# Kernel optimization log

Measured on AMD Instinct MI355X. Metric: run time of the kernel, lower is better.

## Reference

```python
import jax, jax.numpy as jnp
import numpy as np

N_NODES = 20000
N_EDGES = 160000
D = 1000          # out_channels of GatedGraphConv / Linear in-dim
NUM_LAYERS = 3


def setup_inputs() -> dict:
    key = jax.random.key(0)
    ks = jax.random.split(key, 10)
    x = jax.random.normal(ks[0], (N_NODES, D), dtype=jnp.float32)
    edge_index = jax.random.randint(ks[1], (2, N_EDGES), 0, N_NODES, dtype=jnp.int32)
    edge_weight = jax.random.uniform(ks[2], (N_EDGES,), dtype=jnp.float32)
    s = 1.0 / np.sqrt(D)
    weight = jax.random.uniform(ks[3], (NUM_LAYERS, D, D), minval=-s, maxval=s, dtype=jnp.float32)
    w_ih = jax.random.uniform(ks[4], (3 * D, D), minval=-s, maxval=s, dtype=jnp.float32)
    w_hh = jax.random.uniform(ks[5], (3 * D, D), minval=-s, maxval=s, dtype=jnp.float32)
    b_ih = jax.random.uniform(ks[6], (3 * D,), minval=-s, maxval=s, dtype=jnp.float32)
    b_hh = jax.random.uniform(ks[7], (3 * D,), minval=-s, maxval=s, dtype=jnp.float32)
    fc_w = jax.random.uniform(ks[8], (1, D), minval=-s, maxval=s, dtype=jnp.float32)
    fc_b = jax.random.uniform(ks[9], (1,), minval=-s, maxval=s, dtype=jnp.float32)
    return {
        "x": x, "edge_index": edge_index, "edge_weight": edge_weight,
        "weight": weight, "w_ih": w_ih, "w_hh": w_hh, "b_ih": b_ih, "b_hh": b_hh,
        "fc_w": fc_w, "fc_b": fc_b, "prob": 0,
    }


def _gru_cell(m, h, w_ih, w_hh, b_ih, b_hh):
    # torch.nn.GRUCell: gate order r, z, n
    gi = m @ w_ih.T + b_ih   # [N, 3D]
    gh = h @ w_hh.T + b_hh   # [N, 3D]
    i_r, i_z, i_n = jnp.split(gi, 3, axis=-1)
    h_r, h_z, h_n = jnp.split(gh, 3, axis=-1)
    r = jax.nn.sigmoid(i_r + h_r)
    z = jax.nn.sigmoid(i_z + h_z)
    n = jnp.tanh(i_n + r * h_n)
    return (1.0 - z) * n + z * h


def reference(x, edge_index, edge_weight, weight, w_ih, w_hh, b_ih, b_hh, fc_w, fc_b, prob):
    src = edge_index[0]
    dst = edge_index[1]
    h = x
    for layer in range(NUM_LAYERS):
        m = h @ weight[layer]                                  # [N, D]
        msg = m[src] * edge_weight[:, None]                    # [E, D]
        agg = jax.ops.segment_sum(msg, dst, num_segments=N_NODES)  # scatter-add
        h = _gru_cell(agg, h, w_ih, w_hh, b_ih, b_hh)
    h = jax.nn.relu(h)
    # F.dropout with p=prob=0 is identity (scale 1/(1-0)=1)
    return h @ fc_w.T + fc_b                                   # [N, 1]
```

## Files before the change

### kernel.cpp

```cpp
#include <hip/hip_runtime.h>

typedef unsigned short u16;
typedef unsigned int u32;
typedef __attribute__((ext_vector_type(8))) short bf16x8;
typedef __attribute__((ext_vector_type(4))) float f32x4;

#define N_NODES 20000
#define N_EDGES 160000
#define DDIM    1000
#define KP      1024
#define SP      41200000
#define WCAT_L  6291456

__device__ __forceinline__ float b2f(u16 u) {
    union { u32 i; float f; } v; v.i = ((u32)u) << 16; return v.f;
}
__device__ __forceinline__ u16 f2b(float f) {
    union { float f; u32 i; } v; v.f = f;
    u32 r = v.i + 0x7FFFu + ((v.i >> 16) & 1u);
    return (u16)(r >> 16);
}
__device__ __forceinline__ u32 pack2(float a, float b) {
    return (u32)f2b(a) | ((u32)f2b(b) << 16);
}
__device__ __forceinline__ f32x4 mfma16(bf16x8 a, bf16x8 b, f32x4 c) {
    return __builtin_amdgcn_mfma_f32_16x16x32_bf16(a, b, c, 0, 0, 0);
}
__device__ __forceinline__ float fexp_(float x) {
    return __builtin_amdgcn_exp2f(x * 1.4426950408889634f);
}
__device__ __forceinline__ float fsigmoid_(float x) {
    return __builtin_amdgcn_rcpf(1.0f + fexp_(-x));
}
__device__ __forceinline__ float ftanh_(float x) {
    float ax = fabsf(x);
    float e = fexp_(-2.0f * ax);
    float t = (1.0f - e) * __builtin_amdgcn_rcpf(1.0f + e);
    return x >= 0.0f ? t : -t;
}

__device__ __forceinline__ void gl2lds16(const u16* g, u16* l) {
    __builtin_amdgcn_global_load_lds(
        (const __attribute__((address_space(1))) u32*)g,
        (__attribute__((address_space(3))) u32*)l, 16, 0, 0);
}

__global__ __launch_bounds__(256) void cvt_rows(const float* __restrict__ in,
                                                u16* __restrict__ out) {
    int r = blockIdx.x, c = threadIdx.x * 4;
    u32 o[2] = {0, 0};
    if (c < DDIM) {
        float4 v = *(const float4*)(in + (size_t)r * DDIM + c);
        o[0] = pack2(v.x, v.y); o[1] = pack2(v.z, v.w);
    }
    *(uint2*)(out + (size_t)r * KP + c) = *(const uint2*)o;
}

__global__ __launch_bounds__(256) void cvt_weights(const float* __restrict__ wih,
                                                   const float* __restrict__ W,
                                                   const float* __restrict__ whh,
                                                   u16* __restrict__ wihb,
                                                   u16* __restrict__ Wb3,
                                                   u16* __restrict__ wcat) {
    int b = blockIdx.x, c = threadIdx.x * 4;
    const float* src;
    u16* dst;
    if (b < 3000) {
        src = wih + (size_t)b * DDIM;
        dst = wihb + (size_t)b * KP;
    } else if (b < 6000) {
        int r = b - 3000;
        int l = r / 1000, row = r - l * 1000;
        src = W + (size_t)r * DDIM;
        dst = Wb3 + (size_t)l * 1048576 + (size_t)row * KP;
    } else {
        int r = b - 6000;
        int l = r / 3000, gr = r - l * 3000;
        int g = gr / 1000, n2 = gr - g * 1000;
        src = whh + (size_t)gr * DDIM;
        dst = wcat + (size_t)l * WCAT_L + ((size_t)g * 1024 + n2) * 2048 + 1024;
    }
    u32 o[2] = {0, 0};
    if (c < DDIM) {
        float4 v = *(const float4*)(src + c);
        o[0] = pack2(v.x, v.y); o[1] = pack2(v.z, v.w);
    }
    *(uint2*)(dst + c) = *(const uint2*)o;
}

__global__ __launch_bounds__(256) void count_edges(const int* __restrict__ ei,
                                                   int* __restrict__ cnt) {
    int e = blockIdx.x * 256 + threadIdx.x;
    if (e < N_EDGES) atomicAdd(&cnt[ei[N_EDGES + e]], 1);
}

__global__ __launch_bounds__(1024) void scan_offsets(const int* __restrict__ cnt,
                                                     int* __restrict__ ofs) {
    __shared__ int s[1024];
    const int CH = 20;
    int t = threadIdx.x;
    int base = t * CH;
    int loc[CH];
    int sum = 0;
    for (int j = 0; j < CH; j++) {
        int i = base + j;
        loc[j] = sum;
        sum += (i < N_NODES) ? cnt[i] : 0;
    }
    s[t] = sum;
    __syncthreads();
    for (int d = 1; d < 1024; d <<= 1) {
        int v = (t >= d) ? s[t - d] : 0;
        __syncthreads();
        s[t] += v;
        __syncthreads();
    }
    int excl = s[t] - sum;
    for (int j = 0; j < CH; j++) {
        int i = base + j;
        if (i < N_NODES) ofs[i] = excl + loc[j];
    }
    if (t == 0) ofs[N_NODES] = N_EDGES;
}

__global__ __launch_bounds__(256) void fill_buckets(const int* __restrict__ ei,
                                                    const int* __restrict__ ofs,
                                                    int* __restrict__ cur,
                                                    int* __restrict__ bkt) {
    int e = blockIdx.x * 256 + threadIdx.x;
    if (e >= N_EDGES) return;
    int d = ei[N_EDGES + e];
    int pos = atomicAdd(&cur[d], 1);
    bkt[ofs[d] + pos] = e;
}

__global__ __launch_bounds__(256) void node_agg(const int* __restrict__ ei,
                                                const float* __restrict__ ew,
                                                const int* __restrict__ ofs,
                                                const int* __restrict__ bkt,
                                                const u16* __restrict__ hsrc,
                                                u16* __restrict__ agg) {
    __shared__ int   s_src[2][32];
    __shared__ float s_w[2][32];
    __shared__ int   s_it[2];
    int tid = threadIdx.x;
    int half = tid >> 7, t = tid & 127;
    int node = blockIdx.x * 2 + half;
    int beg = ofs[node], end = ofs[node + 1];
    if (t == 0) s_it[half] = (end - beg + 31) >> 5;
    __syncthreads();
    int iters = max(s_it[0], s_it[1]);
    float acc[8] = {};
    for (int it = 0; it < iters; it++) {
        int cb = beg + it * 32;
        int n = min(32, end - cb);
        if (t < n) {
            int e = bkt[cb + t];
            s_src[half][t] = ei[e];
            s_w[half][t]   = ew[e];
        }
        __syncthreads();
        if (t < 125) {
            for (int j = 0; j < n; j++) {
                int src = s_src[half][j];
                float w = s_w[half][j];
                uint4 v = *(const uint4*)(hsrc + (size_t)src * KP + t * 8);
                const u16* p = (const u16*)&v;
#pragma unroll
                for (int k = 0; k < 8; k++) acc[k] += b2f(p[k]) * w;
            }
        }
        __syncthreads();
    }
    if (t < 125) {
        u32 o[4] = {pack2(acc[0], acc[1]), pack2(acc[2], acc[3]),
                    pack2(acc[4], acc[5]), pack2(acc[6], acc[7])};
        *(uint4*)(agg + (size_t)node * KP + t * 8) = *(const uint4*)o;
    } else if (t < 128) {
        uint4 z = {0, 0, 0, 0};
        *(uint4*)(agg + (size_t)node * KP + 1000 + (t - 125) * 8) = z;
    }
}

__global__ __launch_bounds__(256) void gemm_wc(const u16* __restrict__ A,
                                               const u16* __restrict__ Bt3,
                                               u16* __restrict__ wcat) {
    __shared__ u16 S[16384];
    int tid = threadIdx.x;
    int lane = tid & 63, wave = tid >> 6;
    int wr = wave >> 1, wc = wave & 1;
    int bid = blockIdx.x;
    int l = blockIdx.y;
    int m0 = (bid >> 3) * 128, n0 = (bid & 7) * 128;
    const u16* Bt = Bt3 + (size_t)l * 1048576;

    int aoff[4], boff[4];
#pragma unroll
    for (int i = 0; i < 4; i++) {
        int c = tid + 256 * i;
        int row = c >> 3, sl = c & 7;
        int kc = sl ^ (row & 7);
        aoff[i] = (m0 + row) * KP + kc * 8;
        boff[i] = (n0 + row) * KP + kc * 8;
    }
    f32x4 acc[4][4] = {};
    int fr = lane & 15, q = lane >> 4, sw = fr & 7;

    for (int k0 = 0; k0 < KP; k0 += 64) {
#pragma unroll
        for (int i = 0; i < 4; i++) {
            gl2lds16(A + aoff[i] + k0, &S[tid * 8 + 2048 * i]);
            gl2lds16(Bt + boff[i] + k0, &S[8192 + tid * 8 + 2048 * i]);
        }
        __syncthreads();
#pragma unroll
        for (int ks = 0; ks < 2; ks++) {
            int kx = ((ks * 4 + q) ^ sw) * 8;
            bf16x8 af[4], bf[4];
#pragma unroll
            for (int i = 0; i < 4; i++)
                af[i] = *(const bf16x8*)&S[(wr * 64 + i * 16 + fr) * 64 + kx];
#pragma unroll
            for (int j = 0; j < 4; j++)
                bf[j] = *(const bf16x8*)&S[8192 + (wc * 64 + j * 16 + fr) * 64 + kx];
#pragma unroll
            for (int i = 0; i < 4; i++)
#pragma unroll
                for (int j = 0; j < 4; j++)
                    acc[i][j] = mfma16(af[i], bf[j], acc[i][j]);
        }
        __syncthreads();
    }

    u16* wl = wcat + (size_t)l * WCAT_L;
    int cc = lane & 15, r4 = q * 4;
#pragma unroll
    for (int i = 0; i < 4; i++)
#pragma unroll
        for (int j = 0; j < 4; j++) {
            int gn = n0 + wc * 64 + j * 16 + cc;
            if (gn >= DDIM) continue;
#pragma unroll
            for (int r = 0; r < 4; r++) {
                int gm = m0 + wr * 64 + i * 16 + r4 + r;
                if (gm >= 3000) continue;
                int slab = (gm >= 2000) ? 2 : (gm >= 1000 ? 1 : 0);
                int row = gm - slab * 1000;
                wl[(size_t)slab * 2097152 + (size_t)row * 2048 + gn] =
                    f2b(acc[i][j][r]);
            }
        }
}

__global__ __launch_bounds__(512, 2) void gru_fused(const u16* __restrict__ agg,
                                                    const u16* __restrict__ h,
                                                    const u16* __restrict__ wcat,
                                                    const float* __restrict__ bih,
                                                    const float* __restrict__ bhh,
                                                    u16* __restrict__ hout) {
    extern __shared__ u16 S[];
    int tid = threadIdx.x;
    int lane = tid & 63, wave = tid >> 6;
    int wr = wave >> 1, wc = wave & 1;

    int bid = blockIdx.x;
    int xcd = bid & 7;
    int s = bid >> 3;
    int panel = s >> 1, hi = s & 1;
    int m0 = panel * 256;
    int n0 = (xcd * 2 + hi) * 64;

    int aoff[4];
#pragma unroll
    for (int i = 0; i < 4; i++) {
        int c = tid + 512 * i;
        int row = c >> 3, sl = c & 7;
        int kc = sl ^ (row & 7);
        aoff[i] = (m0 + row) * KP + kc * 8;
    }
    int wrow = tid >> 3;
    int woff = (n0 + wrow) * 2048 + ((tid & 7) ^ (wrow & 7)) * 8;

    f32x4 aR[4][2] = {}, aZ[4][2] = {}, aN[4][2] = {}, aH[4][2] = {};
    int fr = lane & 15, q = lane >> 4, sw = fr & 7;
    int kx0 = (q ^ sw) * 8, kx1 = ((4 + q) ^ sw) * 8;
    int arow[4], wcol[2];
#pragma unroll
    for (int i = 0; i < 4; i++) arow[i] = (wr * 64 + i * 16 + fr) * 64;
#pragma unroll
    for (int j = 0; j < 2; j++) wcol[j] = (wc * 32 + j * 16 + fr) * 64;

#define STAGE_W(ts, wb) do {                                                  \
        int kw_ = (ts) * 64;                                                  \
        _Pragma("unroll")                                                     \
        for (int g_ = 0; g_ < 3; g_++)                                        \
            gl2lds16(wcat + (size_t)g_ * 2097152 + woff + kw_,                \
                     &S[49152 + (wb) * 12288 + g_ * 4096 + tid * 8]);         \
    } while (0)

#define STAGE_A2(ts, ab, r0) do {                                             \
        const u16* ap_ = ((ts) < 16) ? agg : h;                               \
        int kb_ = ((ts) < 16) ? (ts) * 64 : (ts) * 64 - 1024;                 \
        _Pragma("unroll")                                                     \
        for (int i_ = (r0); i_ < (r0) + 2; i_++)                              \
            gl2lds16(ap_ + aoff[i_] + kb_,                                    \
                     &S[(ab) * 16384 + tid * 8 + 4096 * i_]);                 \
    } while (0)

#define READ_WF(g_) do {                                                      \
        _Pragma("unroll")                                                     \
        for (int j_ = 0; j_ < 2; j_++) {                                      \
            wf[j_][0] = *(const bf16x8*)&S[Wb + (g_) * 4096 + wcol[j_] + kx0];\
            wf[j_][1] = *(const bf16x8*)&S[Wb + (g_) * 4096 + wcol[j_] + kx1];\
        }                                                                     \
    } while (0)

#define MFMA_G(ACC) do {                                                      \
        _Pragma("unroll")                                                     \
        for (int i_ = 0; i_ < 4; i_++)                                        \
            _Pragma("unroll")                                                 \
            for (int j_ = 0; j_ < 2; j_++) {                                  \
                ACC[i_][j_] = mfma16(af[i_][0], wf[j_][0], ACC[i_][j_]);      \
                ACC[i_][j_] = mfma16(af[i_][1], wf[j_][1], ACC[i_][j_]);      \
            }                                                                 \
    } while (0)

    STAGE_A2(0, 0, 0); STAGE_A2(0, 0, 2);
    STAGE_W(0, 0);
    STAGE_A2(1, 1, 0); STAGE_A2(1, 1, 2);
    asm volatile("s_waitcnt vmcnt(4)" ::: "memory");
    __builtin_amdgcn_s_barrier();

    int abuf = 0;
#pragma unroll 1
    for (int t = 0; t < 32; t++) {
        int Ab = abuf * 16384;
        int Wb = 49152 + (t & 1) * 12288;
        int anext = abuf + 2; if (anext >= 3) anext -= 3;
        bf16x8 af[4][2], wf[2][2];
#pragma unroll
        for (int i = 0; i < 4; i++) {
            af[i][0] = *(const bf16x8*)&S[Ab + arow[i] + kx0];
            af[i][1] = *(const bf16x8*)&S[Ab + arow[i] + kx1];
        }
        READ_WF(0);
        if (t <= 30) STAGE_W(t + 1, (t + 1) & 1);
        MFMA_G(aR);
        READ_WF(1);
        if (t <= 29) STAGE_A2(t + 2, anext, 0);
        MFMA_G(aZ);
        READ_WF(2);
        if (t <= 29) STAGE_A2(t + 2, anext, 2);
        if (t < 16) MFMA_G(aN); else MFMA_G(aH);
        if (t <= 29)      asm volatile("s_waitcnt vmcnt(4)" ::: "memory");
        else if (t == 30) asm volatile("s_waitcnt vmcnt(0)" ::: "memory");
        __builtin_amdgcn_s_barrier();
        abuf++; if (abuf == 3) abuf = 0;
    }
#undef STAGE_W
#undef STAGE_A2
#undef READ_WF
#undef MFMA_G

    int cc = lane & 15, r4 = q * 4;
#pragma unroll
    for (int j = 0; j < 2; j++) {
        int gn = n0 + wc * 32 + j * 16 + cc;
        if (gn >= DDIM) continue;
        float br  = bih[gn] + bhh[gn];
        float bz  = bih[1000 + gn] + bhh[1000 + gn];
        float bni = bih[2000 + gn];
        float bnh = bhh[2000 + gn];
#pragma unroll
        for (int i = 0; i < 4; i++)
#pragma unroll
            for (int r = 0; r < 4; r++) {
                int gm = m0 + wr * 64 + i * 16 + r4 + r;
                if (gm >= N_NODES) continue;
                float rg = fsigmoid_(aR[i][j][r] + br);
                float zg = fsigmoid_(aZ[i][j][r] + bz);
                float ng = ftanh_(aN[i][j][r] + bni + rg * (aH[i][j][r] + bnh));
                size_t idx = (size_t)gm * KP + gn;
                float hp = b2f(h[idx]);
                hout[idx] = f2b((1.0f - zg) * ng + zg * hp);
            }
    }
}

__global__ __launch_bounds__(256) void fc_out(const u16* __restrict__ h,
                                              const float* __restrict__ fw,
                                              const float* __restrict__ fb,
                                              float* __restrict__ out) {
    int row = blockIdx.x * 4 + (threadIdx.x >> 6);
    int lane = threadIdx.x & 63;
    if (row >= N_NODES) return;
    float s = 0.0f;
#pragma unroll
    for (int i = 0; i < 2; i++) {
        int c = lane + 64 * i;
        if (c < 125) {
            uint4 v = *(const uint4*)(h + (size_t)row * KP + c * 8);
            const u16* pv = (const u16*)&v;
            float4 w0 = *(const float4*)(fw + c * 8);
            float4 w1 = *(const float4*)(fw + c * 8 + 4);
            const float* wp = (const float*)&w0;
            float hv;
#pragma unroll
            for (int k = 0; k < 4; k++) {
                hv = b2f(pv[k]);
                s += (hv > 0.0f ? hv : 0.0f) * wp[k];
            }
            wp = (const float*)&w1;
#pragma unroll
            for (int k = 0; k < 4; k++) {
                hv = b2f(pv[4 + k]);
                s += (hv > 0.0f ? hv : 0.0f) * wp[k];
            }
        }
    }
    for (int off = 32; off > 0; off >>= 1) s += __shfl_down(s, off, 64);
    if (lane == 0) out[row] = s + fb[0];
}

extern "C" void kernel_launch(void* const* d_in, const int* in_sizes, int n_in,
                              void* d_out, int out_size, void* d_ws, size_t ws_size,
                              hipStream_t stream) {
    const float* x   = (const float*)d_in[0];
    const int*   ei  = (const int*)d_in[1];
    const float* ew  = (const float*)d_in[2];
    const float* W   = (const float*)d_in[3];
    const float* wih = (const float*)d_in[4];
    const float* whh = (const float*)d_in[5];
    const float* bih = (const float*)d_in[6];
    const float* bhh = (const float*)d_in[7];
    const float* fw  = (const float*)d_in[8];
    const float* fb  = (const float*)d_in[9];
    float* out = (float*)d_out;

    hipFuncSetAttribute((const void*)gru_fused,
                        hipFuncAttributeMaxDynamicSharedMemorySize, 147456);

    char* ws = (char*)d_ws;
    u16* xb   = (u16*)(ws);
    u16* bufA = (u16*)(ws + (size_t)SP);
    u16* bufB = (u16*)(ws + (size_t)2 * SP);
    u16* wcat = (u16*)(ws + 123600000);
    int* cnt  = (int*)(ws + 161400000);
    int* cur  = (int*)(ws + 161480000);
    int* ofs  = (int*)(ws + 161560000);
    int* bkt  = (int*)(ws + 161640192);

    u16* wihb = bufA;
    u16* Wb3  = bufA + 3145728;

    cvt_rows<<<N_NODES, 256, 0, stream>>>(x, xb);
    cvt_weights<<<15000, 256, 0, stream>>>(wih, W, whh, wihb, Wb3, wcat);
    gemm_wc<<<dim3(192, 3), 256, 0, stream>>>(wihb, Wb3, wcat);
    hipMemsetAsync(cnt, 0, 160000, stream);
    count_edges<<<625, 256, 0, stream>>>(ei, cnt);
    scan_offsets<<<1, 1024, 0, stream>>>(cnt, ofs);
    fill_buckets<<<625, 256, 0, stream>>>(ei, ofs, cur, bkt);

    node_agg<<<10000, 256, 0, stream>>>(ei, ew, ofs, bkt, xb, bufB);
    gru_fused<<<1264, 512, 147456, stream>>>(bufB, xb, wcat, bih, bhh, bufA);

    node_agg<<<10000, 256, 0, stream>>>(ei, ew, ofs, bkt, bufA, bufB);
    gru_fused<<<1264, 512, 147456, stream>>>(bufB, bufA, wcat + WCAT_L, bih, bhh, xb);

    node_agg<<<10000, 256, 0, stream>>>(ei, ew, ofs, bkt, xb, bufB);
    gru_fused<<<1264, 512, 147456, stream>>>(bufB, xb, wcat + 2 * WCAT_L, bih, bhh, bufA);

    fc_out<<<5000, 256, 0, stream>>>(bufA, fw, fb, out);
}
```

Before: 1.104 ms.

## Load GRU A-operand fragments directly from global into registers, bypassing LDS

The fused GRU GEMM kernel stops staging the activation (agg/h) tiles through a triple-buffered LDS ring and instead has each lane issue global_load_dwordx4 straight into its MFMA A-fragment registers, one k-step ahead. Only the weight tiles stay double-buffered in LDS, which cuts dynamic shared memory from 147456 to 49152 bytes and removes the LDS write/read round trip for A. The cost is more global/L2 traffic, since rows are no longer shared via LDS across the two wave columns, and a shallower prefetch for A that may expose load latency. Register pressure also rises from holding the prefetched fragments.

```diff
diff --git a/kernel.cpp b/kernel.cpp
--- a/kernel.cpp
+++ b/kernel.cpp
@@ -2,6 +2,7 @@
 
 typedef unsigned short u16;
 typedef unsigned int u32;
+typedef unsigned long long u64;
 typedef __attribute__((ext_vector_type(8))) short bf16x8;
 typedef __attribute__((ext_vector_type(4))) float f32x4;
 
@@ -270,41 +271,41 @@
     int m0 = panel * 256;
     int n0 = (xcd * 2 + hi) * 64;
 
-    int aoff[4];
-#pragma unroll
-    for (int i = 0; i < 4; i++) {
-        int c = tid + 512 * i;
-        int row = c >> 3, sl = c & 7;
-        int kc = sl ^ (row & 7);
-        aoff[i] = (m0 + row) * KP + kc * 8;
-    }
     int wrow = tid >> 3;
     int woff = (n0 + wrow) * 2048 + ((tid & 7) ^ (wrow & 7)) * 8;
 
     f32x4 aR[4][2] = {}, aZ[4][2] = {}, aN[4][2] = {}, aH[4][2] = {};
     int fr = lane & 15, q = lane >> 4, sw = fr & 7;
     int kx0 = (q ^ sw) * 8, kx1 = ((4 + q) ^ sw) * 8;
-    int arow[4], wcol[2];
-#pragma unroll
-    for (int i = 0; i < 4; i++) arow[i] = (wr * 64 + i * 16 + fr) * 64;
+    int wcol[2];
 #pragma unroll
     for (int j = 0; j < 2; j++) wcol[j] = (wc * 32 + j * 16 + fr) * 64;
-
-#define STAGE_W(ts, wb) do {                                                  \
+    u32 aroB[4];
+#pragma unroll
+    for (int i = 0; i < 4; i++)
+        aroB[i] = (u32)(((m0 + wr * 64 + i * 16 + fr) * KP + q * 8) * 2);
+
+    bf16x8 af[4][2];
+
+#define STAGE_W(ts) do {                                                      \
         int kw_ = (ts) * 64;                                                  \
         _Pragma("unroll")                                                     \
         for (int g_ = 0; g_ < 3; g_++)                                        \
             gl2lds16(wcat + (size_t)g_ * 2097152 + woff + kw_,                \
-                     &S[49152 + (wb) * 12288 + g_ * 4096 + tid * 8]);         \
+                     &S[((ts) & 1) * 12288 + g_ * 4096 + tid * 8]);           \
     } while (0)
 
-#define STAGE_A2(ts, ab, r0) do {                                             \
-        const u16* ap_ = ((ts) < 16) ? agg : h;                               \
-        int kb_ = ((ts) < 16) ? (ts) * 64 : (ts) * 64 - 1024;                 \
+#define LOAD_AF(ts) do {                                                      \
+        const u16* ap_ = ((ts) < 16) ? (agg + (ts) * 64)                      \
+                                     : (h + ((ts) * 64 - 1024));              \
         _Pragma("unroll")                                                     \
-        for (int i_ = (r0); i_ < (r0) + 2; i_++)                              \
-            gl2lds16(ap_ + aoff[i_] + kb_,                                    \
-                     &S[(ab) * 16384 + tid * 8 + 4096 * i_]);                 \
+        for (int i_ = 0; i_ < 4; i_++) {                                      \
+            u64 ab_ = (u64)ap_ + aroB[i_];                                    \
+            asm volatile("global_load_dwordx4 %0, %1, off offset:0"           \
+                : "=v"(af[i_][0]) : "v"(ab_) : "memory");                     \
+            asm volatile("global_load_dwordx4 %0, %1, off offset:64"          \
+                : "=v"(af[i_][1]) : "v"(ab_) : "memory");                     \
+        }                                                                     \
     } while (0)
 
 #define READ_WF(g_) do {                                                      \
@@ -325,40 +326,33 @@
             }                                                                 \
     } while (0)
 
-    STAGE_A2(0, 0, 0); STAGE_A2(0, 0, 2);
-    STAGE_W(0, 0);
-    STAGE_A2(1, 1, 0); STAGE_A2(1, 1, 2);
-    asm volatile("s_waitcnt vmcnt(4)" ::: "memory");
+    STAGE_W(0);
+    LOAD_AF(0);
+    asm volatile("s_waitcnt vmcnt(8)" ::: "memory");
     __builtin_amdgcn_s_barrier();
 
-    int abuf = 0;
 #pragma unroll 1
     for (int t = 0; t < 32; t++) {
-        int Ab = abuf * 16384;
-        int Wb = 49152 + (t & 1) * 12288;
-        int anext = abuf + 2; if (anext >= 3) anext -= 3;
-        bf16x8 af[4][2], wf[2][2];
-#pragma unroll
-        for (int i = 0; i < 4; i++) {
-            af[i][0] = *(const bf16x8*)&S[Ab + arow[i] + kx0];
-            af[i][1] = *(const bf16x8*)&S[Ab + arow[i] + kx1];
-        }
+        int Wb = (t & 1) * 12288;
+        if (t <= 30) STAGE_W(t + 1);
+        bf16x8 wf[2][2];
         READ_WF(0);
-        if (t <= 30) STAGE_W(t + 1, (t + 1) & 1);
+        if (t <= 30) asm volatile("s_waitcnt vmcnt(3)" ::: "memory");
+        else         asm volatile("s_waitcnt vmcnt(0)" ::: "memory");
+        __builtin_amdgcn_sched_barrier(0);
         MFMA_G(aR);
         READ_WF(1);
-        if (t <= 29) STAGE_A2(t + 2, anext, 0);
         MFMA_G(aZ);
         READ_WF(2);
-        if (t <= 29) STAGE_A2(t + 2, anext, 2);
         if (t < 16) MFMA_G(aN); else MFMA_G(aH);
-        if (t <= 29)      asm volatile("s_waitcnt vmcnt(4)" ::: "memory");
-        else if (t == 30) asm volatile("s_waitcnt vmcnt(0)" ::: "memory");
-        __builtin_amdgcn_s_barrier();
-        abuf++; if (abuf == 3) abuf = 0;
+        if (t <= 30) {
+            LOAD_AF(t + 1);
+            asm volatile("s_waitcnt vmcnt(8)" ::: "memory");
+            __builtin_amdgcn_s_barrier();
+        }
     }
 #undef STAGE_W
-#undef STAGE_A2
+#undef LOAD_AF
 #undef READ_WF
 #undef MFMA_G
 
@@ -438,7 +432,7 @@
     float* out = (float*)d_out;
 
     hipFuncSetAttribute((const void*)gru_fused,
-                        hipFuncAttributeMaxDynamicSharedMemorySize, 147456);
+                        hipFuncAttributeMaxDynamicSharedMemorySize, 49152);
 
     char* ws = (char*)d_ws;
     u16* xb   = (u16*)(ws);
@@ -462,13 +456,13 @@
     fill_buckets<<<625, 256, 0, stream>>>(ei, ofs, cur, bkt);
 
     node_agg<<<10000, 256, 0, stream>>>(ei, ew, ofs, bkt, xb, bufB);
-    gru_fused<<<1264, 512, 147456, stream>>>(bufB, xb, wcat, bih, bhh, bufA);
+    gru_fused<<<1264, 512, 49152, stream>>>(bufB, xb, wcat, bih, bhh, bufA);
 
     node_agg<<<10000, 256, 0, stream>>>(ei, ew, ofs, bkt, bufA, bufB);
-    gru_fused<<<1264, 512, 147456, stream>>>(bufB, bufA, wcat + WCAT_L, bih, bhh, xb);
+    gru_fused<<<1264, 512, 49152, stream>>>(bufB, bufA, wcat + WCAT_L, bih, bhh, xb);
 
     node_agg<<<10000, 256, 0, stream>>>(ei, ew, ofs, bkt, xb, bufB);
-    gru_fused<<<1264, 512, 147456, stream>>>(bufB, xb, wcat + 2 * WCAT_L, bih, bhh, bufA);
+    gru_fused<<<1264, 512, 49152, stream>>>(bufB, xb, wcat + 2 * WCAT_L, bih, bhh, bufA);
 
     fc_out<<<5000, 256, 0, stream>>>(bufA, fw, fb, out);
 }
```

New measurement: 1.467 ms. 32.8% more time.

## Shrink GRU GEMM tile to 128 rows with 256 threads and double-buffered staging

Applied to the files above, without the earlier changes.

The fused GRU GEMM kernel now uses 128-row M tiles with 4 waves per block instead of 256 rows with 8 waves, doubling the grid and cutting LDS to 80KB. The triple-buffered A / double-buffered W pipeline with fine-grained vmcnt waits is replaced by a simpler double buffer, where A and W for the next k-step are staged together and each step ends in a __syncthreads. The MFMA loop is reordered to load W fragments per gate column inside the gate macro. The aim is better occupancy and load balance, at the cost of less weight reuse per block and coarser synchronisation.

```diff
diff --git a/kernel.cpp b/kernel.cpp
--- a/kernel.cpp
+++ b/kernel.cpp
@@ -2,6 +2,7 @@
 
 typedef unsigned short u16;
 typedef unsigned int u32;
+typedef unsigned long long u64;
 typedef __attribute__((ext_vector_type(8))) short bf16x8;
 typedef __attribute__((ext_vector_type(4))) float f32x4;
 
@@ -252,7 +253,7 @@
         }
 }
 
-__global__ __launch_bounds__(512, 2) void gru_fused(const u16* __restrict__ agg,
+__global__ __launch_bounds__(256, 2) void gru_fused(const u16* __restrict__ agg,
                                                     const u16* __restrict__ h,
                                                     const u16* __restrict__ wcat,
                                                     const float* __restrict__ bih,
@@ -267,19 +268,26 @@
     int xcd = bid & 7;
     int s = bid >> 3;
     int panel = s >> 1, hi = s & 1;
-    int m0 = panel * 256;
+    int m0 = panel * 128;
     int n0 = (xcd * 2 + hi) * 64;
 
     int aoff[4];
 #pragma unroll
     for (int i = 0; i < 4; i++) {
-        int c = tid + 512 * i;
+        int c = tid + 256 * i;
         int row = c >> 3, sl = c & 7;
         int kc = sl ^ (row & 7);
         aoff[i] = (m0 + row) * KP + kc * 8;
     }
-    int wrow = tid >> 3;
-    int woff = (n0 + wrow) * 2048 + ((tid & 7) ^ (wrow & 7)) * 8;
+    int wsrc[6];
+#pragma unroll
+    for (int i = 0; i < 6; i++) {
+        int c = tid + 256 * i;
+        int g = c >> 9, cg = c & 511;
+        int row = cg >> 3, sl = cg & 7;
+        int kc = sl ^ (row & 7);
+        wsrc[i] = g * 2097152 + (n0 + row) * 2048 + kc * 8;
+    }
 
     f32x4 aR[4][2] = {}, aZ[4][2] = {}, aN[4][2] = {}, aH[4][2] = {};
     int fr = lane & 15, q = lane >> 4, sw = fr & 7;
@@ -290,77 +298,53 @@
 #pragma unroll
     for (int j = 0; j < 2; j++) wcol[j] = (wc * 32 + j * 16 + fr) * 64;
 
-#define STAGE_W(ts, wb) do {                                                  \
+#define STAGE_AW(ts) do {                                                     \
+        const u16* ap_ = ((ts) < 16) ? agg : h;                               \
+        int kb_ = ((ts) < 16) ? (ts) * 64 : (ts) * 64 - 1024;                 \
+        int ab_ = ((ts) & 1) * 8192, wb_ = 16384 + ((ts) & 1) * 12288;        \
+        _Pragma("unroll")                                                     \
+        for (int i_ = 0; i_ < 4; i_++)                                        \
+            gl2lds16(ap_ + aoff[i_] + kb_, &S[ab_ + tid * 8 + 2048 * i_]);    \
         int kw_ = (ts) * 64;                                                  \
         _Pragma("unroll")                                                     \
-        for (int g_ = 0; g_ < 3; g_++)                                        \
-            gl2lds16(wcat + (size_t)g_ * 2097152 + woff + kw_,                \
-                     &S[49152 + (wb) * 12288 + g_ * 4096 + tid * 8]);         \
+        for (int i_ = 0; i_ < 6; i_++)                                        \
+            gl2lds16(wcat + wsrc[i_] + kw_, &S[wb_ + tid * 8 + 2048 * i_]);   \
     } while (0)
 
-#define STAGE_A2(ts, ab, r0) do {                                             \
-        const u16* ap_ = ((ts) < 16) ? agg : h;                               \
-        int kb_ = ((ts) < 16) ? (ts) * 64 : (ts) * 64 - 1024;                 \
-        _Pragma("unroll")                                                     \
-        for (int i_ = (r0); i_ < (r0) + 2; i_++)                              \
-            gl2lds16(ap_ + aoff[i_] + kb_,                                    \
-                     &S[(ab) * 16384 + tid * 8 + 4096 * i_]);                 \
-    } while (0)
-
-#define READ_WF(g_) do {                                                      \
+#define GATE(g_, ACC) do {                                                    \
         _Pragma("unroll")                                                     \
         for (int j_ = 0; j_ < 2; j_++) {                                      \
-            wf[j_][0] = *(const bf16x8*)&S[Wb + (g_) * 4096 + wcol[j_] + kx0];\
-            wf[j_][1] = *(const bf16x8*)&S[Wb + (g_) * 4096 + wcol[j_] + kx1];\
+            bf16x8 w0_ = *(const bf16x8*)&S[Wb + (g_) * 4096 + wcol[j_] + kx0];\
+            bf16x8 w1_ = *(const bf16x8*)&S[Wb + (g_) * 4096 + wcol[j_] + kx1];\
+            _Pragma("unroll")                                                 \
+            for (int i_ = 0; i_ < 4; i_++) {                                  \
+                ACC[i_][j_] = mfma16(af[i_][0], w0_, ACC[i_][j_]);            \
+                ACC[i_][j_] = mfma16(af[i_][1], w1_, ACC[i_][j_]);            \
+            }                                                                 \
         }                                                                     \
     } while (0)
 
-#define MFMA_G(ACC) do {                                                      \
-        _Pragma("unroll")                                                     \
-        for (int i_ = 0; i_ < 4; i_++)                                        \
-            _Pragma("unroll")                                                 \
-            for (int j_ = 0; j_ < 2; j_++) {                                  \
-                ACC[i_][j_] = mfma16(af[i_][0], wf[j_][0], ACC[i_][j_]);      \
-                ACC[i_][j_] = mfma16(af[i_][1], wf[j_][1], ACC[i_][j_]);      \
-            }                                                                 \
-    } while (0)
-
-    STAGE_A2(0, 0, 0); STAGE_A2(0, 0, 2);
-    STAGE_W(0, 0);
-    STAGE_A2(1, 1, 0); STAGE_A2(1, 1, 2);
-    asm volatile("s_waitcnt vmcnt(4)" ::: "memory");
-    __builtin_amdgcn_s_barrier();
-
-    int abuf = 0;
+    STAGE_AW(0);
+    __syncthreads();
+
 #pragma unroll 1
     for (int t = 0; t < 32; t++) {
-        int Ab = abuf * 16384;
-        int Wb = 49152 + (t & 1) * 12288;
-        int anext = abuf + 2; if (anext >= 3) anext -= 3;
-        bf16x8 af[4][2], wf[2][2];
+        if (t <= 30) STAGE_AW(t + 1);
+        int Ab = (t & 1) * 8192;
+        int Wb = 16384 + (t & 1) * 12288;
+        bf16x8 af[4][2];
 #pragma unroll
         for (int i = 0; i < 4; i++) {
             af[i][0] = *(const bf16x8*)&S[Ab + arow[i] + kx0];
             af[i][1] = *(const bf16x8*)&S[Ab + arow[i] + kx1];
         }
-        READ_WF(0);
-        if (t <= 30) STAGE_W(t + 1, (t + 1) & 1);
-        MFMA_G(aR);
-        READ_WF(1);
-        if (t <= 29) STAGE_A2(t + 2, anext, 0);
-        MFMA_G(aZ);
-        READ_WF(2);
-        if (t <= 29) STAGE_A2(t + 2, anext, 2);
-        if (t < 16) MFMA_G(aN); else MFMA_G(aH);
-        if (t <= 29)      asm volatile("s_waitcnt vmcnt(4)" ::: "memory");
-        else if (t == 30) asm volatile("s_waitcnt vmcnt(0)" ::: "memory");
-        __builtin_amdgcn_s_barrier();
-        abuf++; if (abuf == 3) abuf = 0;
-    }
-#undef STAGE_W
-#undef STAGE_A2
-#undef READ_WF
-#undef MFMA_G
+        GATE(0, aR);
+        GATE(1, aZ);
+        if (t < 16) GATE(2, aN); else GATE(2, aH);
+        if (t <= 30) __syncthreads();
+    }
+#undef STAGE_AW
+#undef GATE
 
     int cc = lane & 15, r4 = q * 4;
 #pragma unroll
@@ -438,7 +422,7 @@
     float* out = (float*)d_out;
 
     hipFuncSetAttribute((const void*)gru_fused,
-                        hipFuncAttributeMaxDynamicSharedMemorySize, 147456);
+                        hipFuncAttributeMaxDynamicSharedMemorySize, 81920);
 
     char* ws = (char*)d_ws;
     u16* xb   = (u16*)(ws);
@@ -462,13 +446,13 @@
     fill_buckets<<<625, 256, 0, stream>>>(ei, ofs, cur, bkt);
 
     node_agg<<<10000, 256, 0, stream>>>(ei, ew, ofs, bkt, xb, bufB);
-    gru_fused<<<1264, 512, 147456, stream>>>(bufB, xb, wcat, bih, bhh, bufA);
+    gru_fused<<<2512, 256, 81920, stream>>>(bufB, xb, wcat, bih, bhh, bufA);
 
     node_agg<<<10000, 256, 0, stream>>>(ei, ew, ofs, bkt, bufA, bufB);
-    gru_fused<<<1264, 512, 147456, stream>>>(bufB, bufA, wcat + WCAT_L, bih, bhh, xb);
+    gru_fused<<<2512, 256, 81920, stream>>>(bufB, bufA, wcat + WCAT_L, bih, bhh, xb);
 
     node_agg<<<10000, 256, 0, stream>>>(ei, ew, ofs, bkt, xb, bufB);
-    gru_fused<<<1264, 512, 147456, stream>>>(bufB, xb, wcat + 2 * WCAT_L, bih, bhh, bufA);
+    gru_fused<<<2512, 256, 81920, stream>>>(bufB, xb, wcat + 2 * WCAT_L, bih, bhh, bufA);
 
     fc_out<<<5000, 256, 0, stream>>>(bufA, fw, fb, out);
 }
```

Result: no change. 1.124 ms (+1.8%).

## Restructure GRU GEMM main loop with A-fragment register prefetch and MFMA priority

Applied to the files above, without the earlier changes.

The fused GRU gate GEMM loop is reorganized so the next tile's A fragments are read from LDS into registers at the end of each tile, double-buffered across an unrolled-by-two loop. All global-to-LDS stages for a tile are issued up front, and each gate's MFMAs run under raised wave priority with a scheduling barrier. The goal is to hide LDS read latency behind MFMA work. In exchange it uses more registers and waits on all outstanding loads (vmcnt(0)) every tile, which may expose global load latency that the previous partial wait kept hidden.

```diff
diff --git a/kernel.cpp b/kernel.cpp
--- a/kernel.cpp
+++ b/kernel.cpp
@@ -2,6 +2,7 @@
 
 typedef unsigned short u16;
 typedef unsigned int u32;
+typedef unsigned long long u64;
 typedef __attribute__((ext_vector_type(8))) short bf16x8;
 typedef __attribute__((ext_vector_type(4))) float f32x4;
 
@@ -290,77 +291,87 @@
 #pragma unroll
     for (int j = 0; j < 2; j++) wcol[j] = (wc * 32 + j * 16 + fr) * 64;
 
-#define STAGE_W(ts, wb) do {                                                  \
+    bf16x8 afA[4][2], afB[4][2];
+
+#define STAGE_A(ts, slot) do {                                                \
+        const u16* ap_ = ((ts) < 16) ? agg : h;                               \
+        int kb_ = ((ts) < 16) ? (ts) * 64 : (ts) * 64 - 1024;                 \
+        _Pragma("unroll")                                                     \
+        for (int i_ = 0; i_ < 4; i_++)                                        \
+            gl2lds16(ap_ + aoff[i_] + kb_,                                    \
+                     &S[(slot) * 16384 + tid * 8 + 4096 * i_]);               \
+    } while (0)
+
+#define STAGE_W(ts) do {                                                      \
         int kw_ = (ts) * 64;                                                  \
         _Pragma("unroll")                                                     \
         for (int g_ = 0; g_ < 3; g_++)                                        \
             gl2lds16(wcat + (size_t)g_ * 2097152 + woff + kw_,                \
-                     &S[49152 + (wb) * 12288 + g_ * 4096 + tid * 8]);         \
+                     &S[49152 + ((ts) & 1) * 12288 + g_ * 4096 + tid * 8]);   \
     } while (0)
 
-#define STAGE_A2(ts, ab, r0) do {                                             \
-        const u16* ap_ = ((ts) < 16) ? agg : h;                               \
-        int kb_ = ((ts) < 16) ? (ts) * 64 : (ts) * 64 - 1024;                 \
+#define READ_AF(slot, DST) do {                                               \
         _Pragma("unroll")                                                     \
-        for (int i_ = (r0); i_ < (r0) + 2; i_++)                              \
-            gl2lds16(ap_ + aoff[i_] + kb_,                                    \
-                     &S[(ab) * 16384 + tid * 8 + 4096 * i_]);                 \
+        for (int i_ = 0; i_ < 4; i_++) {                                      \
+            DST[i_][0] = *(const bf16x8*)&S[(slot) * 16384 + arow[i_] + kx0]; \
+            DST[i_][1] = *(const bf16x8*)&S[(slot) * 16384 + arow[i_] + kx1]; \
+        }                                                                     \
     } while (0)
 
-#define READ_WF(g_) do {                                                      \
+#define GATE(g_, ACC, AF) do {                                                \
+        bf16x8 w0_[2], w1_[2];                                                \
         _Pragma("unroll")                                                     \
         for (int j_ = 0; j_ < 2; j_++) {                                      \
-            wf[j_][0] = *(const bf16x8*)&S[Wb + (g_) * 4096 + wcol[j_] + kx0];\
-            wf[j_][1] = *(const bf16x8*)&S[Wb + (g_) * 4096 + wcol[j_] + kx1];\
+            w0_[j_] = *(const bf16x8*)&S[Wb + (g_) * 4096 + wcol[j_] + kx0];  \
+            w1_[j_] = *(const bf16x8*)&S[Wb + (g_) * 4096 + wcol[j_] + kx1];  \
         }                                                                     \
+        __builtin_amdgcn_s_setprio(1);                                        \
+        _Pragma("unroll")                                                     \
+        for (int j_ = 0; j_ < 2; j_++)                                        \
+            _Pragma("unroll")                                                 \
+            for (int i_ = 0; i_ < 4; i_++) {                                  \
+                ACC[i_][j_] = mfma16(AF[i_][0], w0_[j_], ACC[i_][j_]);        \
+                ACC[i_][j_] = mfma16(AF[i_][1], w1_[j_], ACC[i_][j_]);        \
+            }                                                                 \
+        __builtin_amdgcn_s_setprio(0);                                        \
     } while (0)
 
-#define MFMA_G(ACC) do {                                                      \
-        _Pragma("unroll")                                                     \
-        for (int i_ = 0; i_ < 4; i_++)                                        \
-            _Pragma("unroll")                                                 \
-            for (int j_ = 0; j_ < 2; j_++) {                                  \
-                ACC[i_][j_] = mfma16(af[i_][0], wf[j_][0], ACC[i_][j_]);      \
-                ACC[i_][j_] = mfma16(af[i_][1], wf[j_][1], ACC[i_][j_]);      \
-            }                                                                 \
+#define TILE(t, AFC, AFN) do {                                                \
+        int s1_ = abuf + 1; if (s1_ >= 3) s1_ -= 3;                           \
+        int s2_ = abuf + 2; if (s2_ >= 3) s2_ -= 3;                           \
+        if ((t) <= 29) STAGE_A((t) + 2, s2_);                                 \
+        if ((t) <= 30) STAGE_W((t) + 1);                                      \
+        int Wb = 49152 + ((t) & 1) * 12288;                                   \
+        GATE(0, aR, AFC);                                                     \
+        GATE(1, aZ, AFC);                                                     \
+        if ((t) < 16) GATE(2, aN, AFC); else GATE(2, aH, AFC);                \
+        __builtin_amdgcn_sched_barrier(0);                                    \
+        if ((t) <= 30) {                                                      \
+            READ_AF(s1_, AFN);                                                \
+            asm volatile("s_waitcnt vmcnt(0)" ::: "memory");                  \
+            __builtin_amdgcn_s_barrier();                                     \
+        }                                                                     \
+        abuf = s1_;                                                           \
     } while (0)
 
-    STAGE_A2(0, 0, 0); STAGE_A2(0, 0, 2);
-    STAGE_W(0, 0);
-    STAGE_A2(1, 1, 0); STAGE_A2(1, 1, 2);
-    asm volatile("s_waitcnt vmcnt(4)" ::: "memory");
+    STAGE_A(0, 0);
+    STAGE_A(1, 1);
+    STAGE_W(0);
+    asm volatile("s_waitcnt vmcnt(0)" ::: "memory");
     __builtin_amdgcn_s_barrier();
+    READ_AF(0, afA);
 
     int abuf = 0;
 #pragma unroll 1
-    for (int t = 0; t < 32; t++) {
-        int Ab = abuf * 16384;
-        int Wb = 49152 + (t & 1) * 12288;
-        int anext = abuf + 2; if (anext >= 3) anext -= 3;
-        bf16x8 af[4][2], wf[2][2];
-#pragma unroll
-        for (int i = 0; i < 4; i++) {
-            af[i][0] = *(const bf16x8*)&S[Ab + arow[i] + kx0];
-            af[i][1] = *(const bf16x8*)&S[Ab + arow[i] + kx1];
-        }
-        READ_WF(0);
-        if (t <= 30) STAGE_W(t + 1, (t + 1) & 1);
-        MFMA_G(aR);
-        READ_WF(1);
-        if (t <= 29) STAGE_A2(t + 2, anext, 0);
-        MFMA_G(aZ);
-        READ_WF(2);
-        if (t <= 29) STAGE_A2(t + 2, anext, 2);
-        if (t < 16) MFMA_G(aN); else MFMA_G(aH);
-        if (t <= 29)      asm volatile("s_waitcnt vmcnt(4)" ::: "memory");
-        else if (t == 30) asm volatile("s_waitcnt vmcnt(0)" ::: "memory");
-        __builtin_amdgcn_s_barrier();
-        abuf++; if (abuf == 3) abuf = 0;
-    }
+    for (int tt = 0; tt < 32; tt += 2) {
+        TILE(tt,     afA, afB);
+        TILE(tt + 1, afB, afA);
+    }
+#undef STAGE_A
 #undef STAGE_W
-#undef STAGE_A2
-#undef READ_WF
-#undef MFMA_G
+#undef READ_AF
+#undef GATE
+#undef TILE
 
     int cc = lane & 15, r4 = q * 4;
 #pragma unroll
```

New measurement: 1.690 ms. +53.1%, slower.
